# Performance work log

Measured on AMD Instinct MI355X. Metric: run time of the kernel, lower is better.

The kernel has to match this reference:

```python
import jax, jax.numpy as jnp
import numpy as np

B, H, W, C = 8, 256, 256, 64
M1, M2 = 32, 32
SCALE = 1.0 / (C * C)


def setup_inputs() -> dict:
    key = jax.random.key(0)
    ku, k1, k2, k3, k4 = jax.random.split(key, 5)
    u = jax.random.normal(ku, (B, H, W, C), dtype=jnp.float32)
    wshape = (C, C, M1, M2)
    w_pos_r = SCALE * jax.random.normal(k1, wshape, dtype=jnp.float32)
    w_pos_i = SCALE * jax.random.normal(k2, wshape, dtype=jnp.float32)
    w_neg_r = SCALE * jax.random.normal(k3, wshape, dtype=jnp.float32)
    w_neg_i = SCALE * jax.random.normal(k4, wshape, dtype=jnp.float32)
    return {"u": u, "w_pos_r": w_pos_r, "w_pos_i": w_pos_i,
            "w_neg_r": w_neg_r, "w_neg_i": w_neg_i}


def _compl_mul2d(inp, weights):
    # inp: [B, m1, m2, Cin] complex; weights: [Cin, Cout, m1, m2] complex
    return jnp.einsum('bxyi,ioxy->bxyo', inp, weights)


def reference(u, w_pos_r, w_pos_i, w_neg_r, w_neg_i):
    b, h, w, c = u.shape
    wf = w // 2 + 1  # rfft size along W
    u_ft = jnp.fft.rfft2(u, axes=(1, 2))  # [B, H, Wf, C] complex
    w_pos = jax.lax.complex(w_pos_r, w_pos_i)
    w_neg = jax.lax.complex(w_neg_r, w_neg_i)
    top = _compl_mul2d(u_ft[:, :M1, :M2, :], w_pos)   # low positive freqs
    bot = _compl_mul2d(u_ft[:, h - M1:, :M2, :], w_neg)  # low negative freqs
    # out_ft zero-initialized, only truncated modes populated.
    # (Original allocates [B,H,W,C] but irfft2 with s=(H,W) only reads
    #  the first W//2+1 columns, which equals this [B,H,Wf,C] tensor.)
    out_ft = jnp.zeros((b, h, wf, c), dtype=u_ft.dtype)
    out_ft = out_ft.at[:, :M1, :M2, :].set(top)
    out_ft = out_ft.at[:, h - M1:, :M2, :].set(bot)
    # out_ft[:, -M1:M1] assignment in original is an empty slice (M1 <= H/2): no-op.
    return jnp.fft.irfft2(out_ft, s=(h, w), axes=(1, 2)).astype(u.dtype)
```

## Files before the change

### kernel.cpp

```cpp
#include <hip/hip_runtime.h>
#include <math.h>

#define BB 8
#define HH 256
#define WW 256
#define CC 64

__device__ inline void cmac(float2& a, float tx, float ty, float2 v) {
    a.x += tx * v.x - ty * v.y;
    a.y += tx * v.y + ty * v.x;
}

__global__ __launch_bounds__(256) void k_tw(float2* __restrict__ Tf,
                                            float2* __restrict__ Ti,
                                            float* __restrict__ Ty,
                                            float* __restrict__ T2) {
    int e = blockIdx.x * 256 + threadIdx.x;
    if (e < 16384) {
        int x = e >> 6;
        int j = e & 63;
        int kxa = j + ((j >> 5) * 192);
        int tt = (kxa * x) & 255;
        float ang = (float)tt * (6.283185307179586f / 256.0f);
        float s, c;
        sincosf(ang, &s, &c);
        Tf[(size_t)x * 64 + j] = make_float2(c, -s);
        const float k = 2.0f / 65536.0f;
        Ti[(size_t)j * 256 + x] = make_float2(c * k, s * k);
    } else {
        int f = e - 16384;
        if (f < 8192) {
            int yp = f >> 6;
            int col = f & 63;
            int par = (col >> 5) & 1;
            int cs = (col >> 4) & 1;
            int m = col & 15;
            int ky = 2 * m + par;
            int tt = (ky * yp) & 255;
            float ang = (float)tt * (6.283185307179586f / 256.0f);
            float s, c;
            sincosf(ang, &s, &c);
            Ty[f] = cs ? -s : c;
        } else {
            int g = f - 8192;
            int pi = g >> 12;
            int j = (g >> 7) & 31;
            int p = g & 127;
            int m = j >> 1, ri = j & 1;
            int ky = 2 * m + pi;
            int tt = (ky * p) & 255;
            float ang = (float)tt * (6.283185307179586f / 256.0f);
            float s, c;
            sincosf(ang, &s, &c);
            T2[g] = ri ? -s : c;
        }
    }
}

__global__ __launch_bounds__(256, 6) void k_fwd_y(const float* __restrict__ u,
                                                  const float* __restrict__ Ty,
                                                  float2* __restrict__ V) {
    __shared__ float ue[32 * 68];
    __shared__ float uo[32 * 68];
    __shared__ float Tt[32 * 68];

    int t = threadIdx.x;
    int b = blockIdx.x >> 8;
    int x = blockIdx.x & 255;
    int i4 = (t & 15) * 4;
    int w = t >> 4;
    int p = w & 1;
    int kyq = w >> 1;
    int yy = t >> 3;
    int c0 = (t & 7) * 8;

    const float* ub = u + ((size_t)(b * HH + x)) * (WW * CC);
    const float* uplane = p ? uo : ue;

    float ar0x=0,ar0y=0,ar0z=0,ar0w=0, ai0x=0,ai0y=0,ai0z=0,ai0w=0;
    float ar1x=0,ar1y=0,ar1z=0,ar1w=0, ai1x=0,ai1y=0,ai1z=0,ai1w=0;

    for (int yt = 0; yt < 4; ++yt) {
        const float* plo = ub + (size_t)(yt * 32 + yy) * CC + c0;
        const float* phi = plo + 128 * CC;
        float4 l0 = *(const float4*)(plo);
        float4 l1 = *(const float4*)(plo + 4);
        float4 h0 = *(const float4*)(phi);
        float4 h1 = *(const float4*)(phi + 4);
        const float* tsrc = Ty + (size_t)(yt * 32 + yy) * 64 + c0;
        float4 t0 = *(const float4*)(tsrc);
        float4 t1 = *(const float4*)(tsrc + 4);

        __syncthreads();
        int wb = yy * 68 + c0;
        *(float4*)(ue + wb)     = make_float4(l0.x + h0.x, l0.y + h0.y, l0.z + h0.z, l0.w + h0.w);
        *(float4*)(ue + wb + 4) = make_float4(l1.x + h1.x, l1.y + h1.y, l1.z + h1.z, l1.w + h1.w);
        *(float4*)(uo + wb)     = make_float4(l0.x - h0.x, l0.y - h0.y, l0.z - h0.z, l0.w - h0.w);
        *(float4*)(uo + wb + 4) = make_float4(l1.x - h1.x, l1.y - h1.y, l1.z - h1.z, l1.w - h1.w);
        *(float4*)(Tt + wb)     = t0;
        *(float4*)(Tt + wb + 4) = t1;
        __syncthreads();

        #pragma unroll
        for (int y2 = 0; y2 < 32; ++y2) {
            const float* tb = Tt + y2 * 68 + p * 32 + kyq * 2;
            float2 cp = *(const float2*)(tb);
            float2 sp = *(const float2*)(tb + 16);
            float4 uq = *(const float4*)(uplane + y2 * 68 + i4);
            ar0x += cp.x * uq.x; ar0y += cp.x * uq.y; ar0z += cp.x * uq.z; ar0w += cp.x * uq.w;
            ai0x += sp.x * uq.x; ai0y += sp.x * uq.y; ai0z += sp.x * uq.z; ai0w += sp.x * uq.w;
            ar1x += cp.y * uq.x; ar1y += cp.y * uq.y; ar1z += cp.y * uq.z; ar1w += cp.y * uq.w;
            ai1x += sp.y * uq.x; ai1y += sp.y * uq.y; ai1z += sp.y * uq.z; ai1w += sp.y * uq.w;
        }
    }

    {
        int ky = 4 * kyq + p;
        float2* vp = V + (size_t)(b * HH + x) * 2048 + ky * 64 + i4;
        *(float4*)(vp)     = make_float4(ar0x, ai0x, ar0y, ai0y);
        *(float4*)(vp + 2) = make_float4(ar0z, ai0z, ar0w, ai0w);
    }
    {
        int ky = 4 * kyq + 2 + p;
        float2* vp = V + (size_t)(b * HH + x) * 2048 + ky * 64 + i4;
        *(float4*)(vp)     = make_float4(ar1x, ai1x, ar1y, ai1y);
        *(float4*)(vp + 2) = make_float4(ar1z, ai1z, ar1w, ai1w);
    }
}

__global__ __launch_bounds__(256) void k_fwd_x(const float2* __restrict__ Tf,
                                               const float2* __restrict__ V,
                                               float2* __restrict__ U) {
    __shared__ float sRe[2 * 2048];
    __shared__ float sIm[2 * 2048];
    __shared__ float2 Ts[32 * 16];

    int bx = blockIdx.x;
    int jq = bx & 3;
    int ky = (bx >> 2) & 31;
    int b  = bx >> 7;
    int t = threadIdx.x;
    int jr = t >> 5;
    int ir = t & 31;

    float2 a00 = {0,0}, a01 = {0,0}, a10 = {0,0}, a11 = {0,0};

    const float2* vb = V + (size_t)b * (HH * 2048) + ky * 64;
    int vrow = t >> 3;
    int vcol = (t & 7) * 8;
    int tjj = (t & 7) * 2;
    int parOff = (jr & 1) * 2048;

    for (int x0 = 0; x0 < 128; x0 += 32) {
        const float2* plo = vb + (size_t)(x0 + vrow) * 2048 + vcol;
        const float2* phi = plo + 128 * 2048;
        float4 l0 = *(const float4*)(plo);
        float4 l1 = *(const float4*)(plo + 2);
        float4 l2 = *(const float4*)(plo + 4);
        float4 l3 = *(const float4*)(plo + 6);
        float4 h0 = *(const float4*)(phi);
        float4 h1 = *(const float4*)(phi + 2);
        float4 h2 = *(const float4*)(phi + 4);
        float4 h3 = *(const float4*)(phi + 6);
        float4 tv = *(const float4*)(Tf + (size_t)(x0 + vrow) * 64 + jq * 16 + tjj);

        __syncthreads();
        *(float4*)&Ts[vrow * 16 + tjj] = tv;
        int wb = vrow * 64 + vcol;
        *(float4*)(sRe + wb)            = make_float4(l0.x+h0.x, l0.z+h0.z, l1.x+h1.x, l1.z+h1.z);
        *(float4*)(sRe + wb + 4)        = make_float4(l2.x+h2.x, l2.z+h2.z, l3.x+h3.x, l3.z+h3.z);
        *(float4*)(sIm + wb)            = make_float4(l0.y+h0.y, l0.w+h0.w, l1.y+h1.y, l1.w+h1.w);
        *(float4*)(sIm + wb + 4)        = make_float4(l2.y+h2.y, l2.w+h2.w, l3.y+h3.y, l3.w+h3.w);
        *(float4*)(sRe + 2048 + wb)     = make_float4(l0.x-h0.x, l0.z-h0.z, l1.x-h1.x, l1.z-h1.z);
        *(float4*)(sRe + 2048 + wb + 4) = make_float4(l2.x-h2.x, l2.z-h2.z, l3.x-h3.x, l3.z-h3.z);
        *(float4*)(sIm + 2048 + wb)     = make_float4(l0.y-h0.y, l0.w-h0.w, l1.y-h1.y, l1.w-h1.w);
        *(float4*)(sIm + 2048 + wb + 4) = make_float4(l2.y-h2.y, l2.w-h2.w, l3.y-h3.y, l3.w-h3.w);
        __syncthreads();

        #pragma unroll
        for (int xx = 0; xx < 32; ++xx) {
            float2 t0 = Ts[xx * 16 + jr];
            float2 t1 = Ts[xx * 16 + jr + 8];
            const float* re = sRe + parOff + xx * 64;
            const float* im = sIm + parOff + xx * 64;
            float vr0 = re[ir], vr1 = re[ir + 32];
            float vi0 = im[ir], vi1 = im[ir + 32];
            a00.x += t0.x*vr0 - t0.y*vi0;  a00.y += t0.x*vi0 + t0.y*vr0;
            a01.x += t0.x*vr1 - t0.y*vi1;  a01.y += t0.x*vi1 + t0.y*vr1;
            a10.x += t1.x*vr0 - t1.y*vi0;  a10.y += t1.x*vi0 + t1.y*vr0;
            a11.x += t1.x*vr1 - t1.y*vi1;  a11.y += t1.x*vi1 + t1.y*vr1;
        }
    }

    int j0 = jq * 16 + jr;
    float2* u0 = U + ((size_t)(j0 * 32 + ky) * 8 + b) * 64 + ir;
    u0[0]  = a00;
    u0[32] = a01;
    float2* u1 = U + ((size_t)((j0 + 8) * 32 + ky) * 8 + b) * 64 + ir;
    u1[0]  = a10;
    u1[32] = a11;
}

__global__ __launch_bounds__(256) void k_modew(const float* __restrict__ wpr,
                                               const float* __restrict__ wpi,
                                               const float* __restrict__ wnr,
                                               const float* __restrict__ wni,
                                               const float2* __restrict__ U,
                                               float2* __restrict__ OF) {
    __shared__ float2 uS[4 * 8 * 64];
    __shared__ float2 wS[4 * 8 * 32];

    int bx = blockIdx.x;
    int j   = bx & 63;
    int kyt = (bx >> 6) & 7;
    int oh  = bx >> 9;
    int ky0 = kyt * 4;
    int sel = j >> 5, kxl = j & 31;
    const float* sr = sel ? wnr : wpr;
    const float* si = sel ? wni : wpi;
    int tid = threadIdx.x;

    const float2* up = U + (size_t)(j * 32 + ky0) * 512;
    #pragma unroll
    for (int k = 0; k < 8; ++k) uS[tid + 256 * k] = up[tid + 256 * k];

    int o32 = tid & 31;
    int bh  = tid >> 5;
    int irS = tid >> 5;
    int ooS = tid & 31;

    float2 acc[4];
    #pragma unroll
    for (int k = 0; k < 4; ++k) acc[k] = make_float2(0.f, 0.f);

    for (int it = 0; it < 8; ++it) {
        __syncthreads();
        {
            int ig = it * 8 + irS;
            int og = oh * 32 + ooS;
            size_t base = (((size_t)(ig * 64 + og)) * 32 + kxl) * 32 + ky0;
            float4 r0 = *(const float4*)(sr + base);
            float4 q0 = *(const float4*)(si + base);
            float2* wrow = wS + irS * 32 + ooS;
            wrow[0 * 256] = make_float2(r0.x, q0.x);
            wrow[1 * 256] = make_float2(r0.y, q0.y);
            wrow[2 * 256] = make_float2(r0.z, q0.z);
            wrow[3 * 256] = make_float2(r0.w, q0.w);
        }
        __syncthreads();
        #pragma unroll
        for (int ir = 0; ir < 8; ++ir) {
            int ig = it * 8 + ir;
            #pragma unroll
            for (int ky = 0; ky < 4; ++ky) {
                float2 wv = wS[ky * 256 + ir * 32 + o32];
                float2 uv = uS[ky * 512 + bh * 64 + ig];
                acc[ky].x += uv.x * wv.x - uv.y * wv.y;
                acc[ky].y += uv.x * wv.y + uv.y * wv.x;
            }
        }
    }

    int og = oh * 32 + o32;
    #pragma unroll
    for (int ky = 0; ky < 4; ++ky) {
        OF[((size_t)(bh * 32 + ky0 + ky) * 64 + j) * 64 + og] = acc[ky];
    }
}

__global__ __launch_bounds__(256) void k_inv_x(const float2* __restrict__ Ti,
                                               const float2* __restrict__ OF,
                                               float2* __restrict__ A) {
    __shared__ float2 Ts[32 * 32];
    __shared__ float2 Os[32 * 64];

    int bx = blockIdx.x;
    int xt = bx & 3;
    int ky = (bx >> 2) & 31;
    int b  = bx >> 7;
    int t = threadIdx.x;
    int or_ = t & 15;
    int xr = t >> 4;

    float2 acc[2][2][4];
    #pragma unroll
    for (int pa = 0; pa < 2; ++pa)
        #pragma unroll
        for (int p = 0; p < 2; ++p)
            #pragma unroll
            for (int q = 0; q < 4; ++q) acc[pa][p][q] = make_float2(0.f, 0.f);

    const float2* ofb = OF + (size_t)(b * 32 + ky) * 4096;
    int sj = t >> 3;
    int sx = (t & 7) * 4;
    int so = (t & 7) * 8;

    for (int kh = 0; kh < 2; ++kh) {
        const float2* tsrc = Ti + (size_t)(kh * 32 + sj) * 256 + xt * 32 + sx;
        float4 t0 = *(const float4*)(tsrc);
        float4 t1 = *(const float4*)(tsrc + 2);
        const float2* osrc = ofb + (size_t)(kh * 32 + sj) * 64 + so;
        float4 o0 = *(const float4*)(osrc);
        float4 o1 = *(const float4*)(osrc + 2);
        float4 o2 = *(const float4*)(osrc + 4);
        float4 o3 = *(const float4*)(osrc + 6);

        __syncthreads();
        *(float4*)&Ts[sj * 32 + sx]     = t0;
        *(float4*)&Ts[sj * 32 + sx + 2] = t1;
        float2* od = &Os[sj * 64 + so];
        *(float4*)(od)     = o0;
        *(float4*)(od + 2) = o1;
        *(float4*)(od + 4) = o2;
        *(float4*)(od + 6) = o3;
        __syncthreads();

        #pragma unroll
        for (int jj = 0; jj < 32; ++jj) {
            float4 tp = *(const float4*)&Ts[jj * 32 + xr * 2];
            float2 q0 = Os[jj * 64 + or_];
            float2 q1 = Os[jj * 64 + or_ + 16];
            float2 q2 = Os[jj * 64 + or_ + 32];
            float2 q3 = Os[jj * 64 + or_ + 48];
            const int pa = jj & 1;
            cmac(acc[pa][0][0], tp.x, tp.y, q0);
            cmac(acc[pa][0][1], tp.x, tp.y, q1);
            cmac(acc[pa][0][2], tp.x, tp.y, q2);
            cmac(acc[pa][0][3], tp.x, tp.y, q3);
            cmac(acc[pa][1][0], tp.z, tp.w, q0);
            cmac(acc[pa][1][1], tp.z, tp.w, q1);
            cmac(acc[pa][1][2], tp.z, tp.w, q2);
            cmac(acc[pa][1][3], tp.z, tp.w, q3);
        }
    }

    float sc = (ky == 0) ? 0.5f : 1.0f;
    #pragma unroll
    for (int p = 0; p < 2; ++p) {
        int x = xt * 32 + xr * 2 + p;
        float2* alo = A + ((size_t)(b * 256 + x) * 32 + ky) * 64 + or_;
        float2* ahi = A + ((size_t)(b * 256 + x + 128) * 32 + ky) * 64 + or_;
        #pragma unroll
        for (int q = 0; q < 4; ++q) {
            float2 se = acc[0][p][q], so2 = acc[1][p][q];
            alo[16 * q] = make_float2((se.x + so2.x) * sc, (se.y + so2.y) * sc);
            ahi[16 * q] = make_float2((se.x - so2.x) * sc, (se.y - so2.y) * sc);
        }
    }
}

__global__ __launch_bounds__(256, 4) void k_inv_y(const float* __restrict__ T2g,
                                                  const float2* __restrict__ A,
                                                  float* __restrict__ out) {
    __shared__ float As[2 * 32 * 64];
    __shared__ float T2s[2 * 8 * 132];

    int t = threadIdx.x;
    int b = blockIdx.x >> 8;
    int x = blockIdx.x & 255;
    int o4 = (t & 15) * 4;
    int pr = t >> 4;

    float acc[2][8][4];
    #pragma unroll
    for (int pi = 0; pi < 2; ++pi)
        #pragma unroll
        for (int pp = 0; pp < 8; ++pp)
            #pragma unroll
            for (int k = 0; k < 4; ++k) acc[pi][pp][k] = 0.f;

    {
        int ky = t >> 3, oc = (t & 7) * 8;
        const float2* ap = A + (size_t)(b * 256 + x) * 2048 + ky * 64 + oc;
        float4 g0 = *(const float4*)(ap);
        float4 g1 = *(const float4*)(ap + 2);
        float4 g2 = *(const float4*)(ap + 4);
        float4 g3 = *(const float4*)(ap + 6);
        int pi = ky & 1, m = ky >> 1;
        float* re = As + ((pi * 32) + 2 * m) * 64 + oc;
        float* im = As + ((pi * 32) + 2 * m + 1) * 64 + oc;
        *(float4*)(re)     = make_float4(g0.x, g0.z, g1.x, g1.z);
        *(float4*)(re + 4) = make_float4(g2.x, g2.z, g3.x, g3.z);
        *(float4*)(im)     = make_float4(g0.y, g0.w, g1.y, g1.w);
        *(float4*)(im + 4) = make_float4(g2.y, g2.w, g3.y, g3.w);
    }

    int pi_s = t >> 7;
    int jj_s = (t >> 4) & 7;
    int pc   = (t & 15) * 8;

    for (int jt = 0; jt < 4; ++jt) {
        const float* tg = T2g + (size_t)(pi_s * 32 + jt * 8 + jj_s) * 128 + pc;
        float4 q0 = *(const float4*)(tg);
        float4 q1 = *(const float4*)(tg + 4);
        __syncthreads();
        float* td = T2s + pi_s * 1056 + jj_s * 132 + pc;
        *(float4*)(td)     = q0;
        *(float4*)(td + 4) = q1;
        __syncthreads();

        #pragma unroll
        for (int pi = 0; pi < 2; ++pi) {
            #pragma unroll
            for (int jj = 0; jj < 8; ++jj) {
                const float* trow = T2s + pi * 1056 + jj * 132 + pr * 8;
                float4 ta = *(const float4*)(trow);
                float4 tb = *(const float4*)(trow + 4);
                const float* arow = As + ((pi * 32) + jt * 8 + jj) * 64 + o4;
                float4 av = *(const float4*)(arow);
                float t8[8] = {ta.x, ta.y, ta.z, ta.w, tb.x, tb.y, tb.z, tb.w};
                #pragma unroll
                for (int pp = 0; pp < 8; ++pp) {
                    acc[pi][pp][0] += t8[pp] * av.x;
                    acc[pi][pp][1] += t8[pp] * av.y;
                    acc[pi][pp][2] += t8[pp] * av.z;
                    acc[pi][pp][3] += t8[pp] * av.w;
                }
            }
        }
    }

    float* op = out + (size_t)(b * 256 + x) * (256 * 64);
    #pragma unroll
    for (int pp = 0; pp < 8; ++pp) {
        int p = pr * 8 + pp;
        float4 lo = make_float4(acc[0][pp][0] + acc[1][pp][0],
                                acc[0][pp][1] + acc[1][pp][1],
                                acc[0][pp][2] + acc[1][pp][2],
                                acc[0][pp][3] + acc[1][pp][3]);
        float4 hi = make_float4(acc[0][pp][0] - acc[1][pp][0],
                                acc[0][pp][1] - acc[1][pp][1],
                                acc[0][pp][2] - acc[1][pp][2],
                                acc[0][pp][3] - acc[1][pp][3]);
        *(float4*)(op + (size_t)p * 64 + o4)         = lo;
        *(float4*)(op + (size_t)(p + 128) * 64 + o4) = hi;
    }
}

extern "C" void kernel_launch(void* const* d_in, const int* in_sizes, int n_in,
                              void* d_out, int out_size, void* d_ws, size_t ws_size,
                              hipStream_t stream) {
    const float* u   = (const float*)d_in[0];
    const float* wpr = (const float*)d_in[1];
    const float* wpi = (const float*)d_in[2];
    const float* wnr = (const float*)d_in[3];
    const float* wni = (const float*)d_in[4];
    float* out = (float*)d_out;

    char* ws = (char*)d_ws;
    float2* U  = (float2*)(ws);
    float2* OF = (float2*)(ws + 8388608);
    float2* V  = (float2*)(ws + 16777216);
    float2* A  = V;
    float2* Tf = (float2*)(ws + 50331648);
    float2* Ti = (float2*)(ws + 50331648 + 131072);
    float*  Ty = (float*)(ws + 50331648 + 262144);
    float*  T2 = (float*)(ws + 50331648 + 262144 + 32768);

    k_tw<<<128, 256, 0, stream>>>(Tf, Ti, Ty, T2);
    k_fwd_y<<<BB * HH, 256, 0, stream>>>(u, Ty, V);
    k_fwd_x<<<1024, 256, 0, stream>>>(Tf, V, U);
    k_modew<<<1024, 256, 0, stream>>>(wpr, wpi, wnr, wni, U, OF);
    k_inv_x<<<1024, 256, 0, stream>>>(Ti, OF, A);
    k_inv_y<<<BB * HH, 256, 0, stream>>>(T2, A, out);
}
```

Measured before the change: 226.6 us.

## Restructure k_inv_y to 512 threads with full twiddle table in shared memory

k_inv_y now launches 512 threads per block, with each thread computing 4 output rows instead of 8. The whole 64x128 twiddle table is loaded into shared memory once, which replaces the four-stage loop that needed a barrier pair per stage, and the As rows are padded to 68 to cut bank conflicts. The k_fwd_y launch bound occupancy hint drops from 6 to 4. The cost is more shared memory per block (about 42KB), which may limit resident blocks, and a smaller per-thread register tile that gives less reuse per shared load.

```diff
diff --git a/kernel.cpp b/kernel.cpp
--- a/kernel.cpp
+++ b/kernel.cpp
@@ -57,7 +57,7 @@
     }
 }
 
-__global__ __launch_bounds__(256, 6) void k_fwd_y(const float* __restrict__ u,
+__global__ __launch_bounds__(256, 4) void k_fwd_y(const float* __restrict__ u,
                                                   const float* __restrict__ Ty,
                                                   float2* __restrict__ V) {
     __shared__ float ue[32 * 68];
@@ -349,11 +349,11 @@
     }
 }
 
-__global__ __launch_bounds__(256, 4) void k_inv_y(const float* __restrict__ T2g,
+__global__ __launch_bounds__(512, 2) void k_inv_y(const float* __restrict__ T2g,
                                                   const float2* __restrict__ A,
                                                   float* __restrict__ out) {
-    __shared__ float As[2 * 32 * 64];
-    __shared__ float T2s[2 * 8 * 132];
+    __shared__ float As[2 * 32 * 68];
+    __shared__ float T2s[2 * 32 * 132];
 
     int t = threadIdx.x;
     int b = blockIdx.x >> 8;
@@ -361,69 +361,63 @@
     int o4 = (t & 15) * 4;
     int pr = t >> 4;
 
-    float acc[2][8][4];
+    float acc[2][4][4];
     #pragma unroll
     for (int pi = 0; pi < 2; ++pi)
         #pragma unroll
-        for (int pp = 0; pp < 8; ++pp)
+        for (int pp = 0; pp < 4; ++pp)
             #pragma unroll
             for (int k = 0; k < 4; ++k) acc[pi][pp][k] = 0.f;
 
     {
-        int ky = t >> 3, oc = (t & 7) * 8;
+        int ky = t >> 4;
+        int oc = (t & 15) * 4;
         const float2* ap = A + (size_t)(b * 256 + x) * 2048 + ky * 64 + oc;
         float4 g0 = *(const float4*)(ap);
         float4 g1 = *(const float4*)(ap + 2);
-        float4 g2 = *(const float4*)(ap + 4);
-        float4 g3 = *(const float4*)(ap + 6);
         int pi = ky & 1, m = ky >> 1;
-        float* re = As + ((pi * 32) + 2 * m) * 64 + oc;
-        float* im = As + ((pi * 32) + 2 * m + 1) * 64 + oc;
-        *(float4*)(re)     = make_float4(g0.x, g0.z, g1.x, g1.z);
-        *(float4*)(re + 4) = make_float4(g2.x, g2.z, g3.x, g3.z);
-        *(float4*)(im)     = make_float4(g0.y, g0.w, g1.y, g1.w);
-        *(float4*)(im + 4) = make_float4(g2.y, g2.w, g3.y, g3.w);
-    }
-
-    int pi_s = t >> 7;
-    int jj_s = (t >> 4) & 7;
-    int pc   = (t & 15) * 8;
-
-    for (int jt = 0; jt < 4; ++jt) {
-        const float* tg = T2g + (size_t)(pi_s * 32 + jt * 8 + jj_s) * 128 + pc;
+        float* re = As + ((pi * 32) + 2 * m) * 68 + oc;
+        float* im = As + ((pi * 32) + 2 * m + 1) * 68 + oc;
+        *(float4*)(re) = make_float4(g0.x, g0.z, g1.x, g1.z);
+        *(float4*)(im) = make_float4(g0.y, g0.w, g1.y, g1.w);
+    }
+    {
+        int row = t >> 3;
+        int c = (t & 7) * 16;
+        const float* tg = T2g + (size_t)row * 128 + c;
         float4 q0 = *(const float4*)(tg);
         float4 q1 = *(const float4*)(tg + 4);
-        __syncthreads();
-        float* td = T2s + pi_s * 1056 + jj_s * 132 + pc;
-        *(float4*)(td)     = q0;
-        *(float4*)(td + 4) = q1;
-        __syncthreads();
-
-        #pragma unroll
-        for (int pi = 0; pi < 2; ++pi) {
-            #pragma unroll
-            for (int jj = 0; jj < 8; ++jj) {
-                const float* trow = T2s + pi * 1056 + jj * 132 + pr * 8;
-                float4 ta = *(const float4*)(trow);
-                float4 tb = *(const float4*)(trow + 4);
-                const float* arow = As + ((pi * 32) + jt * 8 + jj) * 64 + o4;
-                float4 av = *(const float4*)(arow);
-                float t8[8] = {ta.x, ta.y, ta.z, ta.w, tb.x, tb.y, tb.z, tb.w};
-                #pragma unroll
-                for (int pp = 0; pp < 8; ++pp) {
-                    acc[pi][pp][0] += t8[pp] * av.x;
-                    acc[pi][pp][1] += t8[pp] * av.y;
-                    acc[pi][pp][2] += t8[pp] * av.z;
-                    acc[pi][pp][3] += t8[pp] * av.w;
-                }
-            }
+        float4 q2 = *(const float4*)(tg + 8);
+        float4 q3 = *(const float4*)(tg + 12);
+        float* td = T2s + row * 132 + c;
+        *(float4*)(td)      = q0;
+        *(float4*)(td + 4)  = q1;
+        *(float4*)(td + 8)  = q2;
+        *(float4*)(td + 12) = q3;
+    }
+    __syncthreads();
+
+    #pragma unroll
+    for (int pi = 0; pi < 2; ++pi) {
+        #pragma unroll
+        for (int jj = 0; jj < 32; ++jj) {
+            float4 ta = *(const float4*)(T2s + (pi * 32 + jj) * 132 + pr * 4);
+            float4 av = *(const float4*)(As + (pi * 32 + jj) * 68 + o4);
+            acc[pi][0][0] += ta.x * av.x;  acc[pi][0][1] += ta.x * av.y;
+            acc[pi][0][2] += ta.x * av.z;  acc[pi][0][3] += ta.x * av.w;
+            acc[pi][1][0] += ta.y * av.x;  acc[pi][1][1] += ta.y * av.y;
+            acc[pi][1][2] += ta.y * av.z;  acc[pi][1][3] += ta.y * av.w;
+            acc[pi][2][0] += ta.z * av.x;  acc[pi][2][1] += ta.z * av.y;
+            acc[pi][2][2] += ta.z * av.z;  acc[pi][2][3] += ta.z * av.w;
+            acc[pi][3][0] += ta.w * av.x;  acc[pi][3][1] += ta.w * av.y;
+            acc[pi][3][2] += ta.w * av.z;  acc[pi][3][3] += ta.w * av.w;
         }
     }
 
     float* op = out + (size_t)(b * 256 + x) * (256 * 64);
     #pragma unroll
-    for (int pp = 0; pp < 8; ++pp) {
-        int p = pr * 8 + pp;
+    for (int pp = 0; pp < 4; ++pp) {
+        int p = pr * 4 + pp;
         float4 lo = make_float4(acc[0][pp][0] + acc[1][pp][0],
                                 acc[0][pp][1] + acc[1][pp][1],
                                 acc[0][pp][2] + acc[1][pp][2],
@@ -462,5 +456,5 @@
     k_fwd_x<<<1024, 256, 0, stream>>>(Tf, V, U);
     k_modew<<<1024, 256, 0, stream>>>(wpr, wpi, wnr, wni, U, OF);
     k_inv_x<<<1024, 256, 0, stream>>>(Ti, OF, A);
-    k_inv_y<<<BB * HH, 256, 0, stream>>>(T2, A, out);
-}
+    k_inv_y<<<BB * HH, 512, 0, stream>>>(T2, A, out);
+}
```

Measured after the change: 224.3 us. No clear change (-1.0%).
